# Kernel optimization log

Hardware: AMD Instinct MI355X
Metric: run time of the kernel (lower is better)

Reference implementation:

```python
import jax, jax.numpy as jnp
import numpy as np

IN_F, NUM_NODES, OUT_F, H, T = 32, 100000, 8, 64, 4096


def setup_inputs() -> dict:
    key = jax.random.key(0)
    ks = jax.random.split(key, 16)
    s = 1.0 / np.sqrt(H)
    inp = {"x": jax.random.normal(ks[0], (1, T, IN_F), dtype=jnp.float32)}
    # LSTM layer 0 (input size IN_F), layer 1 (input size H); PyTorch gate order i,f,g,o
    inp["w_ih0"] = jax.random.uniform(ks[1], (4 * H, IN_F), minval=-s, maxval=s)
    inp["w_hh0"] = jax.random.uniform(ks[2], (4 * H, H), minval=-s, maxval=s)
    inp["b_ih0"] = jax.random.uniform(ks[3], (4 * H,), minval=-s, maxval=s)
    inp["b_hh0"] = jax.random.uniform(ks[4], (4 * H,), minval=-s, maxval=s)
    inp["w_ih1"] = jax.random.uniform(ks[5], (4 * H, H), minval=-s, maxval=s)
    inp["w_hh1"] = jax.random.uniform(ks[6], (4 * H, H), minval=-s, maxval=s)
    inp["b_ih1"] = jax.random.uniform(ks[7], (4 * H,), minval=-s, maxval=s)
    inp["b_hh1"] = jax.random.uniform(ks[8], (4 * H,), minval=-s, maxval=s)
    # two big projections: hidden_size -> num_nodes * out_features
    D = NUM_NODES * OUT_F
    inp["w_eh"] = jax.random.uniform(ks[9], (D, H), minval=-s, maxval=s)
    inp["b_eh"] = jax.random.uniform(ks[10], (D,), minval=-s, maxval=s)
    inp["w_es"] = jax.random.uniform(ks[11], (D, H), minval=-s, maxval=s)
    inp["b_es"] = jax.random.uniform(ks[12], (D,), minval=-s, maxval=s)
    return inp


def _lstm_layer(xs, w_ih, w_hh, b_ih, b_hh):
    # xs: [T, B, F]; returns outputs [T, B, H] and final (h, c) each [B, H]
    B = xs.shape[1]
    # precompute input contribution for all timesteps (one big GEMM)
    gx = jnp.einsum('tbf,gf->tbg', xs, w_ih) + b_ih + b_hh  # [T, B, 4H]

    def cell(carry, gxt):
        h, c = carry
        g = gxt + h @ w_hh.T  # [B, 4H]
        i, f, gg, o = jnp.split(g, 4, axis=-1)
        c = jax.nn.sigmoid(f) * c + jax.nn.sigmoid(i) * jnp.tanh(gg)
        h = jax.nn.sigmoid(o) * jnp.tanh(c)
        return (h, c), h

    init = (jnp.zeros((B, H), xs.dtype), jnp.zeros((B, H), xs.dtype))
    (h, c), ys = jax.lax.scan(cell, init, gx)
    return ys, h, c


def reference(x, w_ih0, w_hh0, b_ih0, b_hh0, w_ih1, w_hh1, b_ih1, b_hh1,
              w_eh, b_eh, w_es, b_es):
    xs = jnp.transpose(x, (1, 0, 2))  # [T, B, F]
    ys0, _, _ = _lstm_layer(xs, w_ih0, w_hh0, b_ih0, b_hh0)
    _, h1, c1 = _lstm_layer(ys0, w_ih1, w_hh1, b_ih1, b_hh1)
    # final-layer hidden/cell state, each [B, H]; project to num_nodes*out_features
    emb_hidden = h1 @ w_eh.T + b_eh  # [B, NUM_NODES*OUT_F]
    emb_state = c1 @ w_es.T + b_es
    return (emb_state.reshape(-1, NUM_NODES * OUT_F),
            emb_hidden.reshape(-1, NUM_NODES * OUT_F))
```

## Files before the change

### kernel.cpp

```cpp
#include <hip/hip_runtime.h>

#define TT 4096
#define DPROJ 800000

typedef float v2f __attribute__((ext_vector_type(2)));
typedef float v4f __attribute__((ext_vector_type(4)));

__device__ __forceinline__ float fexp2(float x) { return __builtin_amdgcn_exp2f(x); }
__device__ __forceinline__ float frcp(float x) { return __builtin_amdgcn_rcpf(x); }

__device__ __forceinline__ v2f pkfma(v2f a, v2f b, v2f c) {
    asm("v_pk_fma_f32 %0, %1, %2, %0" : "+v"(c) : "v"(a), "v"(b));
    return c;
}

template <int CTRL>
__device__ __forceinline__ float dppf(float x) {
    return __int_as_float(
        __builtin_amdgcn_update_dpp(0, __float_as_int(x), CTRL, 0xF, 0xF, true));
}

__device__ __forceinline__ v2f lo2(v4f v) { return __builtin_shufflevector(v, v, 0, 1); }
__device__ __forceinline__ v2f hi2(v4f v) { return __builtin_shufflevector(v, v, 2, 3); }

__device__ __forceinline__ void barrier_nd() {
    asm volatile("s_waitcnt lgkmcnt(0)\n\ts_barrier" ::: "memory");
}

#define WDECL(nm) v2f nm##0, nm##1, nm##2, nm##3, nm##4, nm##5, nm##6, nm##7;
#define WLOAD(nm, base)                                                      \
    {                                                                        \
        const v4f* q_ = (const v4f*)(base);                                  \
        v4f A_ = q_[0], B_ = q_[1], C_ = q_[2], D_ = q_[3];                  \
        nm##0 = lo2(A_); nm##1 = hi2(A_); nm##2 = lo2(B_); nm##3 = hi2(B_);  \
        nm##4 = lo2(C_); nm##5 = hi2(C_); nm##6 = lo2(D_); nm##7 = hi2(D_);  \
    }
#define WDOT(acc, nm, h)                                                     \
    acc = pkfma(nm##0, h##0, acc); acc = pkfma(nm##1, h##1, acc);            \
    acc = pkfma(nm##2, h##2, acc); acc = pkfma(nm##3, h##3, acc);            \
    acc = pkfma(nm##4, h##4, acc); acc = pkfma(nm##5, h##5, acc);            \
    acc = pkfma(nm##6, h##6, acc); acc = pkfma(nm##7, h##7, acc);
#define HREAD(h, ptr)                                                        \
    v2f h##0, h##1, h##2, h##3, h##4, h##5, h##6, h##7;                      \
    {                                                                        \
        const v4f* p_ = (const v4f*)(ptr);                                   \
        v4f ha_ = p_[0], hb_ = p_[1], hc_ = p_[2], hd_ = p_[3];              \
        h##0 = lo2(ha_); h##1 = hi2(ha_); h##2 = lo2(hb_); h##3 = hi2(hb_);  \
        h##4 = lo2(hc_); h##5 = hi2(hc_); h##6 = lo2(hd_); h##7 = hi2(hd_);  \
    }

#define KEEP8(nm)                                                            \
    asm volatile("" : "+v"(nm##0), "+v"(nm##1), "+v"(nm##2), "+v"(nm##3),    \
                      "+v"(nm##4), "+v"(nm##5), "+v"(nm##6), "+v"(nm##7));

__global__ __launch_bounds__(256) void gx0_kernel(const float* __restrict__ x,
                                                  const float* __restrict__ w_ih0,
                                                  const float* __restrict__ b_ih0,
                                                  const float* __restrict__ b_hh0,
                                                  float* __restrict__ gx0p) {
    __shared__ __align__(16) float xs[32];
    const int t = blockIdx.x;
    const int j = threadIdx.x;
    if (j < 32) xs[j] = x[t * 32 + j];
    __syncthreads();
    const float4* w4 = (const float4*)(w_ih0 + j * 32);
    const float4* x4 = (const float4*)xs;
    float acc = b_ih0[j] + b_hh0[j];
#pragma unroll
    for (int u = 0; u < 8; ++u) {
        float4 w = w4[u];
        float4 xv = x4[u];
        acc += w.x * xv.x + w.y * xv.y + w.z * xv.z + w.w * xv.w;
    }
    const int g = j >> 6;
    const int uu = j & 63;
    gx0p[t * 256 + uu * 4 + g] = acc;
}

__global__ __launch_bounds__(512, 2)
void lstm_kernel(const float* __restrict__ gx0,
                 const float* __restrict__ w_hh0,
                 const float* __restrict__ w_ih1,
                 const float* __restrict__ w_hh1,
                 const float* __restrict__ b_ih1,
                 const float* __restrict__ b_hh1,
                 float* __restrict__ hc_out) {
    __shared__ __align__(16) float lds_pool[24576];
    float(*h0buf)[64] = (float(*)[64])(lds_pool);
    float(*h1buf)[64] = (float(*)[64])(lds_pool + 128);

    const int t = threadIdx.x;
    const int j = t & 255;
    const int u = j >> 2;
    const int q = j & 3;
    const int qk = q * 16;
    const bool qg = (q == 2);
    const float kmul = qg ? -2.885390082f : -1.442695041f;
    const float mm = qg ? 2.0f : 1.0f;
    const float dd = qg ? 1.0f : 0.0f;
    const v2f Z2 = {0.0f, 0.0f};
    float cst = 0.0f;

    if (t < 256) {
        WDECL(wA0_) WDECL(wA1_) WDECL(wA2_) WDECL(wA3_)
        WLOAD(wA0_, w_hh0 + (0 * 64 + u) * 64 + qk)
        WLOAD(wA1_, w_hh0 + (1 * 64 + u) * 64 + qk)
        WLOAD(wA2_, w_hh0 + (2 * 64 + u) * 64 + qk)
        WLOAD(wA3_, w_hh0 + (3 * 64 + u) * 64 + qk)
        const float4* gp = ((const float4*)gx0) + u;
        float4 pf0 = gp[0 * 64];
        float4 pf1 = gp[1 * 64];
        float4 pf2 = gp[2 * 64];
        float4 pf3 = gp[3 * 64];
        if (q == 0) h0buf[1][u] = 0.0f;
        barrier_nd();

#define A_STEP(PF, RDP, WRP, ROWI)                                                      \
    {                                                                                   \
        HREAD(h_, &h0buf[RDP][qk])                                                      \
        v2f a0 = Z2, a1 = Z2, a2 = Z2, a3 = Z2;                                         \
        WDOT(a0, wA0_, h_) WDOT(a1, wA1_, h_) WDOT(a2, wA2_, h_) WDOT(a3, wA3_, h_)     \
        float G0 = a0.x + a0.y, G1 = a1.x + a1.y, G2 = a2.x + a2.y, G3 = a3.x + a3.y;   \
        G0 += dppf<0xB1>(G0); G1 += dppf<0xB1>(G1);                                     \
        G2 += dppf<0xB1>(G2); G3 += dppf<0xB1>(G3);                                     \
        G0 += dppf<0x4E>(G0); G1 += dppf<0x4E>(G1);                                     \
        G2 += dppf<0x4E>(G2); G3 += dppf<0x4E>(G3);                                     \
        G0 += PF.x; G1 += PF.y; G2 += PF.z; G3 += PF.w;                                 \
        float arg = q == 0 ? G0 : (q == 1 ? G1 : (q == 2 ? G2 : G3));                   \
        float act = __builtin_fmaf(mm, frcp(1.0f + fexp2(kmul * arg)), -dd);            \
        float gi = dppf<0x00>(act), gf = dppf<0x55>(act);                               \
        float gg = dppf<0xAA>(act), go = dppf<0xFF>(act);                               \
        cst = __builtin_fmaf(gf, cst, gi * gg);                                         \
        float th = __builtin_fmaf(2.0f, frcp(1.0f + fexp2(-2.885390082f * cst)), -1.0f);\
        float hnew = go * th;                                                           \
        if (q == 0) h0buf[WRP][u] = hnew;                                               \
        PF = gp[(ROWI) * 64];                                                           \
        barrier_nd();                                                                   \
    }

        A_STEP(pf0, 1, 0, 4)
#pragma unroll 1
        for (int b = 0; b < 1023; ++b) {
            KEEP8(wA0_) KEEP8(wA1_) KEEP8(wA2_) KEEP8(wA3_)
            const int i4 = 4 * b;
            A_STEP(pf1, 0, 1, i4 + 5)
            A_STEP(pf2, 1, 0, i4 + 6)
            A_STEP(pf3, 0, 1, i4 + 7)
            A_STEP(pf0, 1, 0, (i4 + 8 < TT ? i4 + 8 : TT - 1))
        }
        A_STEP(pf1, 0, 1, TT - 1)
        A_STEP(pf2, 1, 0, TT - 1)
        A_STEP(pf3, 0, 1, TT - 1)
        barrier_nd();
    } else {
        WDECL(wi0_) WDECL(wi1_) WDECL(wi2_) WDECL(wi3_)
        WDECL(wh0_) WDECL(wh1_) WDECL(wh2_) WDECL(wh3_)
        WLOAD(wi0_, w_ih1 + (0 * 64 + u) * 64 + qk)
        WLOAD(wi1_, w_ih1 + (1 * 64 + u) * 64 + qk)
        WLOAD(wi2_, w_ih1 + (2 * 64 + u) * 64 + qk)
        WLOAD(wi3_, w_ih1 + (3 * 64 + u) * 64 + qk)
        WLOAD(wh0_, w_hh1 + (0 * 64 + u) * 64 + qk)
        WLOAD(wh1_, w_hh1 + (1 * 64 + u) * 64 + qk)
        WLOAD(wh2_, w_hh1 + (2 * 64 + u) * 64 + qk)
        WLOAD(wh3_, w_hh1 + (3 * 64 + u) * 64 + qk)
        float4 bias;
        bias.x = b_ih1[0 * 64 + u] + b_hh1[0 * 64 + u];
        bias.y = b_ih1[1 * 64 + u] + b_hh1[1 * 64 + u];
        bias.z = b_ih1[2 * 64 + u] + b_hh1[2 * 64 + u];
        bias.w = b_ih1[3 * 64 + u] + b_hh1[3 * 64 + u];
        float hlast = 0.0f;
        if (q == 0) h1buf[1][u] = 0.0f;
        barrier_nd();
        barrier_nd();

#define B_STEP(P)                                                                       \
    {                                                                                   \
        HREAD(h_, &h0buf[P][qk])                                                        \
        HREAD(k_, &h1buf[(P) ^ 1][qk])                                                  \
        v2f a0 = Z2, a1 = Z2, a2 = Z2, a3 = Z2;                                         \
        v2f c0 = Z2, c1 = Z2, c2 = Z2, c3 = Z2;                                         \
        WDOT(a0, wi0_, h_) WDOT(a1, wi1_, h_) WDOT(a2, wi2_, h_) WDOT(a3, wi3_, h_)     \
        WDOT(c0, wh0_, k_) WDOT(c1, wh1_, k_) WDOT(c2, wh2_, k_) WDOT(c3, wh3_, k_)     \
        float G0 = (a0.x + a0.y) + (c0.x + c0.y);                                       \
        float G1 = (a1.x + a1.y) + (c1.x + c1.y);                                       \
        float G2 = (a2.x + a2.y) + (c2.x + c2.y);                                       \
        float G3 = (a3.x + a3.y) + (c3.x + c3.y);                                       \
        G0 += dppf<0xB1>(G0); G1 += dppf<0xB1>(G1);                                     \
        G2 += dppf<0xB1>(G2); G3 += dppf<0xB1>(G3);                                     \
        G0 += dppf<0x4E>(G0); G1 += dppf<0x4E>(G1);                                     \
        G2 += dppf<0x4E>(G2); G3 += dppf<0x4E>(G3);                                     \
        G0 += bias.x; G1 += bias.y; G2 += bias.z; G3 += bias.w;                         \
        float arg = q == 0 ? G0 : (q == 1 ? G1 : (q == 2 ? G2 : G3));                   \
        float act = __builtin_fmaf(mm, frcp(1.0f + fexp2(kmul * arg)), -dd);            \
        float gi = dppf<0x00>(act), gf = dppf<0x55>(act);                               \
        float gg = dppf<0xAA>(act), go = dppf<0xFF>(act);                               \
        cst = __builtin_fmaf(gf, cst, gi * gg);                                         \
        float th = __builtin_fmaf(2.0f, frcp(1.0f + fexp2(-2.885390082f * cst)), -1.0f);\
        float hnew = go * th;                                                           \
        hlast = hnew;                                                                   \
        if (q == 0) h1buf[P][u] = hnew;                                                 \
        barrier_nd();                                                                   \
    }

#pragma unroll 1
        for (int b = 0; b < 1023; ++b) {
            KEEP8(wi0_) KEEP8(wi1_) KEEP8(wi2_) KEEP8(wi3_)
            KEEP8(wh0_) KEEP8(wh1_) KEEP8(wh2_) KEEP8(wh3_)
            asm volatile("" : "+v"(bias.x), "+v"(bias.y), "+v"(bias.z), "+v"(bias.w));
            B_STEP(0)
            B_STEP(1)
            B_STEP(0)
            B_STEP(1)
        }
        B_STEP(0)
        B_STEP(1)
        B_STEP(0)
        B_STEP(1)
        if (q == 0) {
            hc_out[u] = hlast;
            hc_out[64 + u] = cst;
        }
    }
}

__global__ __launch_bounds__(256) void proj_kernel(const float* __restrict__ hc,
                                                   const float* __restrict__ w_es,
                                                   const float* __restrict__ b_es,
                                                   const float* __restrict__ w_eh,
                                                   const float* __restrict__ b_eh,
                                                   float* __restrict__ out) {
    __shared__ __align__(16) float hv[64];
    __shared__ __align__(16) float cv[64];
    const int tid = threadIdx.x;
    if (tid < 64) hv[tid] = hc[tid];
    else if (tid < 128) cv[tid - 64] = hc[tid];
    __syncthreads();

    const int p = tid & 3;
    const long r = (long)blockIdx.x * 64 + (tid >> 2);
    const float* w;
    const float* bb;
    const float* v;
    long rr;
    if (r < DPROJ) {
        rr = r;
        w = w_es;
        bb = b_es;
        v = cv;
    } else {
        rr = r - DPROJ;
        w = w_eh;
        bb = b_eh;
        v = hv;
    }
    const float4* wp = (const float4*)(w + rr * 64 + p * 16);
    const float4* vp = (const float4*)(v + p * 16);
    v2f s = {0.0f, 0.0f};
#pragma unroll
    for (int cc = 0; cc < 4; ++cc) {
        float4 wv = wp[cc];
        float4 vv = vp[cc];
        v2f w01 = {wv.x, wv.y}, v01 = {vv.x, vv.y};
        v2f w23 = {wv.z, wv.w}, v23 = {vv.z, vv.w};
        s = pkfma(w01, v01, s);
        s = pkfma(w23, v23, s);
    }
    float sum = s.x + s.y;
    sum += dppf<0xB1>(sum);
    sum += dppf<0x4E>(sum);
    if (p == 0) out[r] = sum + bb[rr];
}

extern "C" void kernel_launch(void* const* d_in, const int* in_sizes, int n_in,
                              void* d_out, int out_size, void* d_ws, size_t ws_size,
                              hipStream_t stream) {
    const float* x = (const float*)d_in[0];
    const float* w_ih0 = (const float*)d_in[1];
    const float* w_hh0 = (const float*)d_in[2];
    const float* b_ih0 = (const float*)d_in[3];
    const float* b_hh0 = (const float*)d_in[4];
    const float* w_ih1 = (const float*)d_in[5];
    const float* w_hh1 = (const float*)d_in[6];
    const float* b_ih1 = (const float*)d_in[7];
    const float* b_hh1 = (const float*)d_in[8];
    const float* w_eh = (const float*)d_in[9];
    const float* b_eh = (const float*)d_in[10];
    const float* w_es = (const float*)d_in[11];
    const float* b_es = (const float*)d_in[12];
    float* out = (float*)d_out;

    float* gx0 = (float*)d_ws;
    float* hc = gx0 + 4096 * 256;

    gx0_kernel<<<4096, 256, 0, stream>>>(x, w_ih0, b_ih0, b_hh0, gx0);
    lstm_kernel<<<1, 512, 0, stream>>>(gx0, w_hh0, w_ih1, w_hh1, b_ih1, b_hh1, hc);
    proj_kernel<<<2 * DPROJ / 64, 256, 0, stream>>>(hc, w_es, b_es, w_eh, b_eh, out);
}
```

Measured before the change: 2.355 ms.

## Split layer-1 input projection into a third pipelined wavegroup stage

Adds a third group of 256 threads that computes the layer-1 input-gate contribution (w_ih1 · h0) one step behind layer 0 and passes it through LDS to the layer-1 recurrence group. The layer-1 group then only does the w_hh1 recurrent dot product per step, which shortens its critical path and frees registers. In exchange the pipeline gets one more stage of latency, the block grows to 768 threads, and the register-pinning asm hints are removed, which may change register allocation.

Measured after the change: 2.325 ms. No clear change (-1.3%).

```diff
diff --git a/kernel.cpp b/kernel.cpp
--- a/kernel.cpp
+++ b/kernel.cpp
@@ -48,10 +48,6 @@
         h##0 = lo2(ha_); h##1 = hi2(ha_); h##2 = lo2(hb_); h##3 = hi2(hb_);  \
         h##4 = lo2(hc_); h##5 = hi2(hc_); h##6 = lo2(hd_); h##7 = hi2(hd_);  \
     }
-
-#define KEEP8(nm)                                                            \
-    asm volatile("" : "+v"(nm##0), "+v"(nm##1), "+v"(nm##2), "+v"(nm##3),    \
-                      "+v"(nm##4), "+v"(nm##5), "+v"(nm##6), "+v"(nm##7));
 
 __global__ __launch_bounds__(256) void gx0_kernel(const float* __restrict__ x,
                                                   const float* __restrict__ w_ih0,
@@ -77,7 +73,7 @@
     gx0p[t * 256 + uu * 4 + g] = acc;
 }
 
-__global__ __launch_bounds__(512, 2)
+__global__ __launch_bounds__(768, 3)
 void lstm_kernel(const float* __restrict__ gx0,
                  const float* __restrict__ w_hh0,
                  const float* __restrict__ w_ih1,
@@ -88,8 +84,10 @@
     __shared__ __align__(16) float lds_pool[24576];
     float(*h0buf)[64] = (float(*)[64])(lds_pool);
     float(*h1buf)[64] = (float(*)[64])(lds_pool + 128);
+    float(*pbuf)[256] = (float(*)[256])(lds_pool + 256);
 
     const int t = threadIdx.x;
+    const int g3 = t >> 8;
     const int j = t & 255;
     const int u = j >> 2;
     const int q = j & 3;
@@ -101,7 +99,7 @@
     const v2f Z2 = {0.0f, 0.0f};
     float cst = 0.0f;
 
-    if (t < 256) {
+    if (g3 == 0) {
         WDECL(wA0_) WDECL(wA1_) WDECL(wA2_) WDECL(wA3_)
         WLOAD(wA0_, w_hh0 + (0 * 64 + u) * 64 + qk)
         WLOAD(wA1_, w_hh0 + (1 * 64 + u) * 64 + qk)
@@ -141,7 +139,6 @@
         A_STEP(pf0, 1, 0, 4)
 #pragma unroll 1
         for (int b = 0; b < 1023; ++b) {
-            KEEP8(wA0_) KEEP8(wA1_) KEEP8(wA2_) KEEP8(wA3_)
             const int i4 = 4 * b;
             A_STEP(pf1, 0, 1, i4 + 5)
             A_STEP(pf2, 1, 0, i4 + 6)
@@ -152,45 +149,64 @@
         A_STEP(pf2, 1, 0, TT - 1)
         A_STEP(pf3, 0, 1, TT - 1)
         barrier_nd();
+        barrier_nd();
+    } else if (g3 == 1) {
+        WDECL(wC0_) WDECL(wC1_) WDECL(wC2_) WDECL(wC3_)
+        WLOAD(wC0_, w_ih1 + (0 * 64 + u) * 64 + qk)
+        WLOAD(wC1_, w_ih1 + (1 * 64 + u) * 64 + qk)
+        WLOAD(wC2_, w_ih1 + (2 * 64 + u) * 64 + qk)
+        WLOAD(wC3_, w_ih1 + (3 * 64 + u) * 64 + qk)
+        barrier_nd();
+        barrier_nd();
+
+#define C_STEP(RD)                                                                      \
+    {                                                                                   \
+        HREAD(h_, &h0buf[RD][qk])                                                       \
+        v2f a0 = Z2, a1 = Z2, a2 = Z2, a3 = Z2;                                         \
+        WDOT(a0, wC0_, h_) WDOT(a1, wC1_, h_) WDOT(a2, wC2_, h_) WDOT(a3, wC3_, h_)     \
+        float G0 = a0.x + a0.y, G1 = a1.x + a1.y, G2 = a2.x + a2.y, G3 = a3.x + a3.y;   \
+        G0 += dppf<0xB1>(G0); G1 += dppf<0xB1>(G1);                                     \
+        G2 += dppf<0xB1>(G2); G3 += dppf<0xB1>(G3);                                     \
+        G0 += dppf<0x4E>(G0); G1 += dppf<0x4E>(G1);                                     \
+        G2 += dppf<0x4E>(G2); G3 += dppf<0x4E>(G3);                                     \
+        float val = q == 0 ? G0 : (q == 1 ? G1 : (q == 2 ? G2 : G3));                   \
+        pbuf[RD][j] = val;                                                              \
+        barrier_nd();                                                                   \
+    }
+
+#pragma unroll 1
+        for (int b = 0; b < 1024; ++b) {
+            C_STEP(0)
+            C_STEP(1)
+            C_STEP(0)
+            C_STEP(1)
+        }
+        barrier_nd();
     } else {
-        WDECL(wi0_) WDECL(wi1_) WDECL(wi2_) WDECL(wi3_)
         WDECL(wh0_) WDECL(wh1_) WDECL(wh2_) WDECL(wh3_)
-        WLOAD(wi0_, w_ih1 + (0 * 64 + u) * 64 + qk)
-        WLOAD(wi1_, w_ih1 + (1 * 64 + u) * 64 + qk)
-        WLOAD(wi2_, w_ih1 + (2 * 64 + u) * 64 + qk)
-        WLOAD(wi3_, w_ih1 + (3 * 64 + u) * 64 + qk)
         WLOAD(wh0_, w_hh1 + (0 * 64 + u) * 64 + qk)
         WLOAD(wh1_, w_hh1 + (1 * 64 + u) * 64 + qk)
         WLOAD(wh2_, w_hh1 + (2 * 64 + u) * 64 + qk)
         WLOAD(wh3_, w_hh1 + (3 * 64 + u) * 64 + qk)
-        float4 bias;
-        bias.x = b_ih1[0 * 64 + u] + b_hh1[0 * 64 + u];
-        bias.y = b_ih1[1 * 64 + u] + b_hh1[1 * 64 + u];
-        bias.z = b_ih1[2 * 64 + u] + b_hh1[2 * 64 + u];
-        bias.w = b_ih1[3 * 64 + u] + b_hh1[3 * 64 + u];
+        const float biasq = b_ih1[q * 64 + u] + b_hh1[q * 64 + u];
         float hlast = 0.0f;
         if (q == 0) h1buf[1][u] = 0.0f;
         barrier_nd();
         barrier_nd();
+        barrier_nd();
 
 #define B_STEP(P)                                                                       \
     {                                                                                   \
-        HREAD(h_, &h0buf[P][qk])                                                        \
         HREAD(k_, &h1buf[(P) ^ 1][qk])                                                  \
-        v2f a0 = Z2, a1 = Z2, a2 = Z2, a3 = Z2;                                         \
+        float pv = pbuf[P][j];                                                          \
         v2f c0 = Z2, c1 = Z2, c2 = Z2, c3 = Z2;                                         \
-        WDOT(a0, wi0_, h_) WDOT(a1, wi1_, h_) WDOT(a2, wi2_, h_) WDOT(a3, wi3_, h_)     \
         WDOT(c0, wh0_, k_) WDOT(c1, wh1_, k_) WDOT(c2, wh2_, k_) WDOT(c3, wh3_, k_)     \
-        float G0 = (a0.x + a0.y) + (c0.x + c0.y);                                       \
-        float G1 = (a1.x + a1.y) + (c1.x + c1.y);                                       \
-        float G2 = (a2.x + a2.y) + (c2.x + c2.y);                                       \
-        float G3 = (a3.x + a3.y) + (c3.x + c3.y);                                       \
+        float G0 = c0.x + c0.y, G1 = c1.x + c1.y, G2 = c2.x + c2.y, G3 = c3.x + c3.y;   \
         G0 += dppf<0xB1>(G0); G1 += dppf<0xB1>(G1);                                     \
         G2 += dppf<0xB1>(G2); G3 += dppf<0xB1>(G3);                                     \
         G0 += dppf<0x4E>(G0); G1 += dppf<0x4E>(G1);                                     \
         G2 += dppf<0x4E>(G2); G3 += dppf<0x4E>(G3);                                     \
-        G0 += bias.x; G1 += bias.y; G2 += bias.z; G3 += bias.w;                         \
-        float arg = q == 0 ? G0 : (q == 1 ? G1 : (q == 2 ? G2 : G3));                   \
+        float arg = (q == 0 ? G0 : (q == 1 ? G1 : (q == 2 ? G2 : G3))) + pv + biasq;    \
         float act = __builtin_fmaf(mm, frcp(1.0f + fexp2(kmul * arg)), -dd);            \
         float gi = dppf<0x00>(act), gf = dppf<0x55>(act);                               \
         float gg = dppf<0xAA>(act), go = dppf<0xFF>(act);                               \
@@ -203,19 +219,12 @@
     }
 
 #pragma unroll 1
-        for (int b = 0; b < 1023; ++b) {
-            KEEP8(wi0_) KEEP8(wi1_) KEEP8(wi2_) KEEP8(wi3_)
-            KEEP8(wh0_) KEEP8(wh1_) KEEP8(wh2_) KEEP8(wh3_)
-            asm volatile("" : "+v"(bias.x), "+v"(bias.y), "+v"(bias.z), "+v"(bias.w));
+        for (int b = 0; b < 1024; ++b) {
             B_STEP(0)
             B_STEP(1)
             B_STEP(0)
             B_STEP(1)
         }
-        B_STEP(0)
-        B_STEP(1)
-        B_STEP(0)
-        B_STEP(1)
         if (q == 0) {
             hc_out[u] = hlast;
             hc_out[64 + u] = cst;
@@ -293,6 +302,6 @@
     float* hc = gx0 + 4096 * 256;
 
     gx0_kernel<<<4096, 256, 0, stream>>>(x, w_ih0, b_ih0, b_hh0, gx0);
-    lstm_kernel<<<1, 512, 0, stream>>>(gx0, w_hh0, w_ih1, w_hh1, b_ih1, b_hh1, hc);
+    lstm_kernel<<<1, 768, 0, stream>>>(gx0, w_hh0, w_ih1, w_hh1, b_ih1, b_hh1, hc);
     proj_kernel<<<2 * DPROJ / 64, 256, 0, stream>>>(hc, w_es, b_es, w_eh, b_eh, out);
 }
```
